# Kernel optimization log

Hardware: AMD Instinct MI355X
Metric: run time of the kernel (lower is better)

## Reference

```python
import math
import jax, jax.numpy as jnp
import numpy as np
from jax import lax

INPUT_SIZE = 736
PATCH_SIZE = 16
PATCH_LENGTH = 768
EMBED_DIM = 768
BATCH = 32
N_RINGS = INPUT_SIZE // 2  # 368 rings, equal_interval=1


def _precompute_gather(input_size=INPUT_SIZE, patch_length=PATCH_LENGTH):
    """Replicates the torch buffer construction: per-radius-ring pixel masks
    sorted by angle, fused with the per-ring linear (align_corners=True)
    resize to patch_length. Returns flat gather indices and lerp weights."""
    H = W = input_size
    yc = np.arange(H) - (H - 1) / 2.0
    xc = np.arange(W) - (W - 1) / 2.0
    yy, xx = np.meshgrid(yc, xc, indexing='ij')  # yy=row offset, xx=col offset
    radius = np.sqrt(xx ** 2 + yy ** 2)
    R = input_size // 2
    off = (W - 1) / 2.0
    j = np.arange(patch_length)
    idx0_all, idx1_all, w_all = [], [], []
    for low in range(R):
        high = low + 1
        m = (radius > low) & (radius <= high)
        ry, rx = np.nonzero(m)  # row-major order, same as torch .nonzero()
        # Faithful to torch quirk: unbind names (x, y) = (row-off, col-off)
        xv = ry - off
        yv = rx - off
        deg = np.arctan2(-yv, xv) * 180.0 / math.pi
        flat = ry * W + rx
        order = np.argsort(deg, kind='stable')
        flat = flat[order]
        L = len(flat)
        # F.interpolate(mode='linear', align_corners=True) to patch_length
        if L == 1:
            src = np.zeros(patch_length)
        else:
            src = j * (L - 1) / (patch_length - 1)
        i0 = np.clip(np.floor(src).astype(np.int64), 0, L - 1)
        i1 = np.minimum(i0 + 1, L - 1)
        wt = (src - i0).astype(np.float32)
        idx0_all.append(flat[i0])
        idx1_all.append(flat[i1])
        w_all.append(wt)
    idx0 = np.concatenate(idx0_all).astype(np.int32)
    idx1 = np.concatenate(idx1_all).astype(np.int32)
    w = np.concatenate(w_all).astype(np.float32)
    return idx0, idx1, w


def setup_inputs() -> dict:
    key = jax.random.key(0)
    k1, k2 = jax.random.split(key)
    x = jax.random.normal(k1, (BATCH, 3, INPUT_SIZE, INPUT_SIZE), dtype=jnp.float32)
    fan_in = 3 * PATCH_SIZE * PATCH_SIZE
    conv_w = jax.random.normal(k2, (EMBED_DIM, 3, PATCH_SIZE, PATCH_SIZE), dtype=jnp.float32) / np.sqrt(fan_in)
    conv_b = jnp.zeros((EMBED_DIM,), dtype=jnp.float32)
    idx0, idx1, w = _precompute_gather()
    return {
        'x': x,
        'conv_w': conv_w,
        'conv_b': conv_b,
        'idx0': jnp.asarray(idx0),
        'idx1': jnp.asarray(idx1),
        'w': jnp.asarray(w),
    }


def reference(x, conv_w, conv_b, idx0, idx1, w):
    N = x.shape[0]
    flat = x.reshape(N, 3, -1)  # [N, 3, H*W]
    # Fused irregular gather + per-ring linear resize (lerp between neighbors)
    g0 = flat[:, :, idx0]
    g1 = flat[:, :, idx1]
    patches = g0 * (1.0 - w) + g1 * w  # [N, 3, N_RINGS*PATCH_LENGTH]
    patches = patches.reshape(N, 3, N_RINGS, PATCH_LENGTH)  # [N,3,368,768]
    out = lax.conv_general_dilated(
        patches, conv_w,
        window_strides=(PATCH_SIZE, PATCH_SIZE),
        padding='VALID',
        dimension_numbers=('NCHW', 'OIHW', 'NCHW'),
    )
    return out + conv_b[None, :, None, None]  # [N, 768, 23, 48]
```

## Files before the change

### kernel.cpp

```cpp
#include <hip/hip_runtime.h>
#include <hip/hip_bf16.h>
#include <stdint.h>

#define INPUT_SIZE   736
#define PLANE_ELEMS  (736*736)
#define N_RINGS      368
#define PATCH_LEN    768
#define EMBED        768
#define BATCH        32
#define KDIM         768
#define M_TOTAL      (BATCH*23*48)
#define P_PER_BATCH  1104
#define OUT_BATCH_STRIDE 847872

typedef __bf16 bf16x8 __attribute__((ext_vector_type(8)));
typedef float  floatx4 __attribute__((ext_vector_type(4)));

__global__ void wcast_kernel(const float* __restrict__ wsrc,
                             __hip_bfloat16* __restrict__ Wb) {
    int i = blockIdx.x * 256 + threadIdx.x;
    Wb[i] = __float2bfloat16(wsrc[i]);
}

__global__ void gather_kernel(const float* __restrict__ x,
                              const int*   __restrict__ idx0,
                              const int*   __restrict__ idx1,
                              const float* __restrict__ w,
                              __hip_bfloat16* __restrict__ A) {
    int b    = blockIdx.x;
    int half = b & 1;
    int bb   = b >> 1;
    int band = bb % 23;
    int nc   = bb / 23;
    int c    = nc % 3;
    int n    = nc / 3;
    const float* plane = x + (size_t)nc * PLANE_ELEMS;

    int rr = threadIdx.x >> 4;
    int jj = threadIdx.x & 15;
    int r  = band * 16 + rr;
    int tbase = r * PATCH_LEN + jj + half * (24 * 16);
    size_t abase = ((size_t)(n * P_PER_BATCH + band * 48 + half * 24)) * KDIM
                 + c * 256 + threadIdx.x;

    #pragma unroll 8
    for (int jc = 0; jc < 24; jc++) {
        int t  = tbase + jc * 16;
        int i0 = idx0[t];
        int i1 = idx1[t];
        float wt = w[t];
        float v  = plane[i0] * (1.0f - wt) + plane[i1] * wt;
        A[abase + (size_t)jc * KDIM] = __float2bfloat16(v);
    }
}

__global__ __launch_bounds__(256) void gemm_kernel(
        const __hip_bfloat16* __restrict__ A,
        const __hip_bfloat16* __restrict__ Wb,
        const float* __restrict__ cb,
        float* __restrict__ out)
{
    __shared__ __hip_bfloat16 As[128 * 32];
    __shared__ __hip_bfloat16 Bs[128 * 32];

    const int tid  = threadIdx.x;
    const int lane = tid & 63;
    const int wv   = tid >> 6;
    const int wm   = wv & 1;
    const int wn   = wv >> 1;
    const int quad = lane >> 4;
    const int l16  = lane & 15;

    const int bn = blockIdx.x;
    const int bm = blockIdx.y;

    floatx4 acc[4][4];
    #pragma unroll
    for (int i = 0; i < 4; i++)
        #pragma unroll
        for (int j = 0; j < 4; j++)
            acc[i][j] = (floatx4){0.f, 0.f, 0.f, 0.f};

    const int srow = tid >> 2;
    const int kofs = (tid & 3) * 8;
    const __hip_bfloat16* aSrc = A  + (size_t)(bm * 128 + srow) * KDIM + kofs;
    const __hip_bfloat16* bSrc = Wb + (size_t)(bn * 128 + srow) * KDIM + kofs;
    __hip_bfloat16* aDst = As + tid * 8;
    __hip_bfloat16* bDst = Bs + tid * 8;

    for (int kt = 0; kt < 24; kt++) {
        const __hip_bfloat16* ap = aSrc + kt * 32;
        const __hip_bfloat16* bp = bSrc + kt * 32;
        __builtin_amdgcn_global_load_lds(
            (const __attribute__((address_space(1))) void*)(const void*)ap,
            (__attribute__((address_space(3))) void*)(void*)aDst, 16, 0, 0);
        __builtin_amdgcn_global_load_lds(
            (const __attribute__((address_space(1))) void*)(const void*)(ap + (size_t)64 * KDIM),
            (__attribute__((address_space(3))) void*)(void*)(aDst + 64 * 32), 16, 0, 0);
        __builtin_amdgcn_global_load_lds(
            (const __attribute__((address_space(1))) void*)(const void*)bp,
            (__attribute__((address_space(3))) void*)(void*)bDst, 16, 0, 0);
        __builtin_amdgcn_global_load_lds(
            (const __attribute__((address_space(1))) void*)(const void*)(bp + (size_t)64 * KDIM),
            (__attribute__((address_space(3))) void*)(void*)(bDst + 64 * 32), 16, 0, 0);
        __syncthreads();

        bf16x8 af[4], bfr[4];
        #pragma unroll
        for (int mi = 0; mi < 4; mi++) {
            int ml = wm * 64 + mi * 16 + l16;
            af[mi] = *(const bf16x8*)(As + ml * 32 + quad * 8);
        }
        #pragma unroll
        for (int ni = 0; ni < 4; ni++) {
            int el = wn * 64 + ni * 16 + l16;
            bfr[ni] = *(const bf16x8*)(Bs + el * 32 + quad * 8);
        }
        #pragma unroll
        for (int mi = 0; mi < 4; mi++)
            #pragma unroll
            for (int ni = 0; ni < 4; ni++)
                acc[mi][ni] = __builtin_amdgcn_mfma_f32_16x16x32_bf16(
                                  af[mi], bfr[ni], acc[mi][ni], 0, 0, 0);
        __syncthreads();
    }

    const int m0 = bm * 128 + wm * 64;
    const int e0 = bn * 128 + wn * 64;
    #pragma unroll
    for (int ni = 0; ni < 4; ni++) {
        int eg = e0 + ni * 16 + l16;
        float bias = cb[eg];
        #pragma unroll
        for (int mi = 0; mi < 4; mi++) {
            int mg = m0 + mi * 16 + quad * 4;
            int nb = mg / P_PER_BATCH;
            int p  = mg - nb * P_PER_BATCH;
            floatx4 v = acc[mi][ni];
            v[0] += bias; v[1] += bias; v[2] += bias; v[3] += bias;
            *(floatx4*)(out + (size_t)nb * OUT_BATCH_STRIDE
                            + (size_t)eg * P_PER_BATCH + p) = v;
        }
    }
}

extern "C" void kernel_launch(void* const* d_in, const int* in_sizes, int n_in,
                              void* d_out, int out_size, void* d_ws, size_t ws_size,
                              hipStream_t stream) {
    const float* x      = (const float*)d_in[0];
    const float* conv_w = (const float*)d_in[1];
    const float* conv_b = (const float*)d_in[2];
    const int*   idx0   = (const int*)  d_in[3];
    const int*   idx1   = (const int*)  d_in[4];
    const float* w      = (const float*)d_in[5];
    float* out = (float*)d_out;

    __hip_bfloat16* A  = (__hip_bfloat16*)d_ws;
    __hip_bfloat16* Wb = A + (size_t)M_TOTAL * KDIM;

    wcast_kernel<<<dim3(EMBED * KDIM / 256), dim3(256), 0, stream>>>(conv_w, Wb);

    gather_kernel<<<dim3(BATCH * 3 * (N_RINGS / 16) * 2), dim3(256), 0, stream>>>(
        x, idx0, idx1, w, A);

    gemm_kernel<<<dim3(EMBED / 128, M_TOTAL / 128), dim3(256), 0, stream>>>(
        A, Wb, conv_b, out);
}
```

Baseline: 444.4 us.

## Pack gather indices and weights into int2 and vectorize gather stores

Adds a pre-pass that packs idx0, the idx1-idx0 delta and a 16-bit quantized weight into one int2 per tap. The gather kernel then reads two taps per 16-byte load instead of three separate streams, and writes two bf16 values per store. This cuts index-metadata traffic, which repeats for every batch and channel. It adds an extra kernel launch and quantizes the lerp weight to 16 bits, a small accuracy change.

New measurement: 452.1 us. About the same (+1.7%).

```diff
diff --git a/kernel.cpp b/kernel.cpp
--- a/kernel.cpp
+++ b/kernel.cpp
@@ -12,9 +12,15 @@
 #define M_TOTAL      (BATCH*23*48)
 #define P_PER_BATCH  1104
 #define OUT_BATCH_STRIDE 847872
+#define GATHER_T     (N_RINGS*PATCH_LEN)
 
 typedef __bf16 bf16x8 __attribute__((ext_vector_type(8)));
 typedef float  floatx4 __attribute__((ext_vector_type(4)));
+
+static __device__ __forceinline__ unsigned short bf16bits(float f) {
+    __hip_bfloat16 h = __float2bfloat16(f);
+    return *reinterpret_cast<unsigned short*>(&h);
+}
 
 __global__ void wcast_kernel(const float* __restrict__ wsrc,
                              __hip_bfloat16* __restrict__ Wb) {
@@ -22,10 +28,20 @@
     Wb[i] = __float2bfloat16(wsrc[i]);
 }
 
+__global__ void pack_kernel(const int*   __restrict__ idx0,
+                            const int*   __restrict__ idx1,
+                            const float* __restrict__ w,
+                            int2* __restrict__ P) {
+    int t = blockIdx.x * 256 + threadIdx.x;
+    int i0 = idx0[t];
+    int d  = idx1[t] - i0;
+    unsigned w16 = (unsigned)(w[t] * 65536.0f);
+    if (w16 > 65535u) w16 = 65535u;
+    P[t] = make_int2(i0, (int)((w16 << 16) | ((unsigned)d & 0xFFFFu)));
+}
+
 __global__ void gather_kernel(const float* __restrict__ x,
-                              const int*   __restrict__ idx0,
-                              const int*   __restrict__ idx1,
-                              const float* __restrict__ w,
+                              const int2*  __restrict__ P,
                               __hip_bfloat16* __restrict__ A) {
     int b    = blockIdx.x;
     int half = b & 1;
@@ -39,18 +55,25 @@
     int rr = threadIdx.x >> 4;
     int jj = threadIdx.x & 15;
     int r  = band * 16 + rr;
-    int tbase = r * PATCH_LEN + jj + half * (24 * 16);
-    size_t abase = ((size_t)(n * P_PER_BATCH + band * 48 + half * 24)) * KDIM
-                 + c * 256 + threadIdx.x;
+    int tbase = r * PATCH_LEN + half * 384 + jj * 2;
 
-    #pragma unroll 8
-    for (int jc = 0; jc < 24; jc++) {
-        int t  = tbase + jc * 16;
-        int i0 = idx0[t];
-        int i1 = idx1[t];
-        float wt = w[t];
-        float v  = plane[i0] * (1.0f - wt) + plane[i1] * wt;
-        A[abase + (size_t)jc * KDIM] = __float2bfloat16(v);
+    int k = c * 256 + rr * 16 + (jj & 7) * 2;
+    size_t mbase = (size_t)(n * P_PER_BATCH + band * 48 + half * 24 + (jj >> 3));
+    __hip_bfloat16* aptr = A + mbase * KDIM + k;
+
+    #pragma unroll 4
+    for (int it = 0; it < 12; it++) {
+        int4 q = *reinterpret_cast<const int4*>(&P[tbase + it * 32]);
+        int   i0a = q.x;
+        int   i1a = i0a + (int)(short)((unsigned)q.y & 0xFFFFu);
+        float wa  = (float)((unsigned)q.y >> 16) * (1.0f / 65536.0f);
+        float va  = plane[i0a] * (1.0f - wa) + plane[i1a] * wa;
+        int   i0b = q.z;
+        int   i1b = i0b + (int)(short)((unsigned)q.w & 0xFFFFu);
+        float wb  = (float)((unsigned)q.w >> 16) * (1.0f / 65536.0f);
+        float vb  = plane[i0b] * (1.0f - wb) + plane[i1b] * wb;
+        *reinterpret_cast<ushort2*>(aptr + (size_t)(it * 2) * KDIM) =
+            make_ushort2(bf16bits(va), bf16bits(vb));
     }
 }
 
@@ -157,11 +180,14 @@
 
     __hip_bfloat16* A  = (__hip_bfloat16*)d_ws;
     __hip_bfloat16* Wb = A + (size_t)M_TOTAL * KDIM;
+    int2*           P  = (int2*)(Wb + (size_t)EMBED * KDIM);
 
     wcast_kernel<<<dim3(EMBED * KDIM / 256), dim3(256), 0, stream>>>(conv_w, Wb);
 
+    pack_kernel<<<dim3(GATHER_T / 256), dim3(256), 0, stream>>>(idx0, idx1, w, P);
+
     gather_kernel<<<dim3(BATCH * 3 * (N_RINGS / 16) * 2), dim3(256), 0, stream>>>(
-        x, idx0, idx1, w, A);
+        x, P, A);
 
     gemm_kernel<<<dim3(EMBED / 128, M_TOTAL / 128), dim3(256), 0, stream>>>(
         A, Wb, conv_b, out);
```

## Fuse ring gather and patch-embedding GEMM into one kernel via LDS

Applied to the files above, without the earlier changes.

Merges the gather/lerp kernel and the GEMM into one kernel. Each block owns one batch and one 16-row band, gathers its 48x768 A tile straight into swizzled LDS, then runs MFMA against bf16 weights read directly from global memory. This removes the write and re-read of the bf16 A matrix through HBM and one launch. The cost is only 736 blocks, 72 KB of LDS per block limiting occupancy, and B fragments loaded from global/L2 without LDS staging.

After: 477.2 us. 1.07x slower.

```diff
diff --git a/kernel.cpp b/kernel.cpp
--- a/kernel.cpp
+++ b/kernel.cpp
@@ -9,12 +9,16 @@
 #define EMBED        768
 #define BATCH        32
 #define KDIM         768
-#define M_TOTAL      (BATCH*23*48)
 #define P_PER_BATCH  1104
 #define OUT_BATCH_STRIDE 847872
 
 typedef __bf16 bf16x8 __attribute__((ext_vector_type(8)));
 typedef float  floatx4 __attribute__((ext_vector_type(4)));
+
+static __device__ __forceinline__ unsigned short bf16bits(float f) {
+    __hip_bfloat16 h = __float2bfloat16(f);
+    return *reinterpret_cast<unsigned short*>(&h);
+}
 
 __global__ void wcast_kernel(const float* __restrict__ wsrc,
                              __hip_bfloat16* __restrict__ Wb) {
@@ -22,124 +26,106 @@
     Wb[i] = __float2bfloat16(wsrc[i]);
 }
 
-__global__ void gather_kernel(const float* __restrict__ x,
-                              const int*   __restrict__ idx0,
-                              const int*   __restrict__ idx1,
-                              const float* __restrict__ w,
-                              __hip_bfloat16* __restrict__ A) {
-    int b    = blockIdx.x;
-    int half = b & 1;
-    int bb   = b >> 1;
-    int band = bb % 23;
-    int nc   = bb / 23;
-    int c    = nc % 3;
-    int n    = nc / 3;
-    const float* plane = x + (size_t)nc * PLANE_ELEMS;
-
-    int rr = threadIdx.x >> 4;
-    int jj = threadIdx.x & 15;
-    int r  = band * 16 + rr;
-    int tbase = r * PATCH_LEN + jj + half * (24 * 16);
-    size_t abase = ((size_t)(n * P_PER_BATCH + band * 48 + half * 24)) * KDIM
-                 + c * 256 + threadIdx.x;
-
-    #pragma unroll 8
-    for (int jc = 0; jc < 24; jc++) {
-        int t  = tbase + jc * 16;
-        int i0 = idx0[t];
-        int i1 = idx1[t];
-        float wt = w[t];
-        float v  = plane[i0] * (1.0f - wt) + plane[i1] * wt;
-        A[abase + (size_t)jc * KDIM] = __float2bfloat16(v);
-    }
-}
-
-__global__ __launch_bounds__(256) void gemm_kernel(
-        const __hip_bfloat16* __restrict__ A,
+__global__ __launch_bounds__(512, 4) void fused_kernel(
+        const float* __restrict__ x,
+        const int*   __restrict__ idx0,
+        const int*   __restrict__ idx1,
+        const float* __restrict__ w,
         const __hip_bfloat16* __restrict__ Wb,
         const float* __restrict__ cb,
         float* __restrict__ out)
 {
-    __shared__ __hip_bfloat16 As[128 * 32];
-    __shared__ __hip_bfloat16 Bs[128 * 32];
+    __shared__ __hip_bfloat16 Alds[48 * 768];
 
+    const int n    = blockIdx.x;
+    const int band = blockIdx.y;
     const int tid  = threadIdx.x;
+
+    {
+        const int rr    = tid & 15;
+        const int jslot = tid >> 4;
+        const int r     = band * 16 + rr;
+        const float* pl0 = x + (size_t)(n * 3 + 0) * PLANE_ELEMS;
+        const float* pl1 = x + (size_t)(n * 3 + 1) * PLANE_ELEMS;
+        const float* pl2 = x + (size_t)(n * 3 + 2) * PLANE_ELEMS;
+
+        #pragma unroll 2
+        for (int it = 0; it < 12; it++) {
+            const int j0 = jslot * 2 + it * 64;
+            const int t  = r * PATCH_LEN + j0;
+            int2   i0p = *(const int2*)(idx0 + t);
+            int2   i1p = *(const int2*)(idx1 + t);
+            float2 wp  = *(const float2*)(w + t);
+            const int pl  = j0 >> 4;
+            const int klo = j0 & 15;
+
+            #pragma unroll
+            for (int c = 0; c < 3; c++) {
+                const float* pp = (c == 0) ? pl0 : (c == 1) ? pl1 : pl2;
+                float va = pp[i0p.x] * (1.0f - wp.x) + pp[i1p.x] * wp.x;
+                float vb = pp[i0p.y] * (1.0f - wp.y) + pp[i1p.y] * wp.y;
+                const int k  = c * 256 + rr * 16 + klo;
+                const int s8 = k >> 3;
+                const int sw = (s8 & ~7) | ((s8 ^ pl) & 7);
+                *(ushort2*)((unsigned short*)Alds + pl * 768 + sw * 8 + (k & 7))
+                    = make_ushort2(bf16bits(va), bf16bits(vb));
+            }
+        }
+    }
+    __syncthreads();
+
     const int lane = tid & 63;
     const int wv   = tid >> 6;
-    const int wm   = wv & 1;
-    const int wn   = wv >> 1;
     const int quad = lane >> 4;
     const int l16  = lane & 15;
 
-    const int bn = blockIdx.x;
-    const int bm = blockIdx.y;
+    float* outBase = out + (size_t)n * OUT_BATCH_STRIDE + band * 48;
 
-    floatx4 acc[4][4];
     #pragma unroll
-    for (int i = 0; i < 4; i++)
+    for (int pass = 0; pass < 2; pass++) {
+        const int e0w = pass * 384 + wv * 48;
+
+        floatx4 acc[3][3];
         #pragma unroll
-        for (int j = 0; j < 4; j++)
-            acc[i][j] = (floatx4){0.f, 0.f, 0.f, 0.f};
+        for (int i = 0; i < 3; i++)
+            #pragma unroll
+            for (int j = 0; j < 3; j++)
+                acc[i][j] = (floatx4){0.f, 0.f, 0.f, 0.f};
 
-    const int srow = tid >> 2;
-    const int kofs = (tid & 3) * 8;
-    const __hip_bfloat16* aSrc = A  + (size_t)(bm * 128 + srow) * KDIM + kofs;
-    const __hip_bfloat16* bSrc = Wb + (size_t)(bn * 128 + srow) * KDIM + kofs;
-    __hip_bfloat16* aDst = As + tid * 8;
-    __hip_bfloat16* bDst = Bs + tid * 8;
+        #pragma unroll 2
+        for (int kt = 0; kt < 24; kt++) {
+            bf16x8 af[3], bfr[3];
+            const int s8 = kt * 4 + quad;
+            #pragma unroll
+            for (int mt = 0; mt < 3; mt++) {
+                const int row = mt * 16 + l16;
+                const int sw  = (s8 & ~7) | ((s8 ^ row) & 7);
+                af[mt] = *(const bf16x8*)(Alds + row * 768 + sw * 8);
+            }
+            #pragma unroll
+            for (int ni = 0; ni < 3; ni++) {
+                const int e = e0w + ni * 16 + l16;
+                bfr[ni] = *(const bf16x8*)(Wb + (size_t)e * KDIM + kt * 32 + quad * 8);
+            }
+            #pragma unroll
+            for (int mt = 0; mt < 3; mt++)
+                #pragma unroll
+                for (int ni = 0; ni < 3; ni++)
+                    acc[mt][ni] = __builtin_amdgcn_mfma_f32_16x16x32_bf16(
+                                      af[mt], bfr[ni], acc[mt][ni], 0, 0, 0);
+        }
 
-    for (int kt = 0; kt < 24; kt++) {
-        const __hip_bfloat16* ap = aSrc + kt * 32;
-        const __hip_bfloat16* bp = bSrc + kt * 32;
-        __builtin_amdgcn_global_load_lds(
-            (const __attribute__((address_space(1))) void*)(const void*)ap,
-            (__attribute__((address_space(3))) void*)(void*)aDst, 16, 0, 0);
-        __builtin_amdgcn_global_load_lds(
-            (const __attribute__((address_space(1))) void*)(const void*)(ap + (size_t)64 * KDIM),
-            (__attribute__((address_space(3))) void*)(void*)(aDst + 64 * 32), 16, 0, 0);
-        __builtin_amdgcn_global_load_lds(
-            (const __attribute__((address_space(1))) void*)(const void*)bp,
-            (__attribute__((address_space(3))) void*)(void*)bDst, 16, 0, 0);
-        __builtin_amdgcn_global_load_lds(
-            (const __attribute__((address_space(1))) void*)(const void*)(bp + (size_t)64 * KDIM),
-            (__attribute__((address_space(3))) void*)(void*)(bDst + 64 * 32), 16, 0, 0);
-        __syncthreads();
-
-        bf16x8 af[4], bfr[4];
         #pragma unroll
-        for (int mi = 0; mi < 4; mi++) {
-            int ml = wm * 64 + mi * 16 + l16;
-            af[mi] = *(const bf16x8*)(As + ml * 32 + quad * 8);
-        }
-        #pragma unroll
-        for (int ni = 0; ni < 4; ni++) {
-            int el = wn * 64 + ni * 16 + l16;
-            bfr[ni] = *(const bf16x8*)(Bs + el * 32 + quad * 8);
-        }
-        #pragma unroll
-        for (int mi = 0; mi < 4; mi++)
+        for (int ni = 0; ni < 3; ni++) {
+            const int eg = e0w + ni * 16 + l16;
+            const float bias = cb[eg];
             #pragma unroll
-            for (int ni = 0; ni < 4; ni++)
-                acc[mi][ni] = __builtin_amdgcn_mfma_f32_16x16x32_bf16(
-                                  af[mi], bfr[ni], acc[mi][ni], 0, 0, 0);
-        __syncthreads();
-    }
-
-    const int m0 = bm * 128 + wm * 64;
-    const int e0 = bn * 128 + wn * 64;
-    #pragma unroll
-    for (int ni = 0; ni < 4; ni++) {
-        int eg = e0 + ni * 16 + l16;
-        float bias = cb[eg];
-        #pragma unroll
-        for (int mi = 0; mi < 4; mi++) {
-            int mg = m0 + mi * 16 + quad * 4;
-            int nb = mg / P_PER_BATCH;
-            int p  = mg - nb * P_PER_BATCH;
-            floatx4 v = acc[mi][ni];
-            v[0] += bias; v[1] += bias; v[2] += bias; v[3] += bias;
-            *(floatx4*)(out + (size_t)nb * OUT_BATCH_STRIDE
-                            + (size_t)eg * P_PER_BATCH + p) = v;
+            for (int mt = 0; mt < 3; mt++) {
+                const int pl = mt * 16 + quad * 4;
+                floatx4 v = acc[mt][ni];
+                v[0] += bias; v[1] += bias; v[2] += bias; v[3] += bias;
+                *(floatx4*)(outBase + (size_t)eg * P_PER_BATCH + pl) = v;
+            }
         }
     }
 }
@@ -155,14 +141,10 @@
     const float* w      = (const float*)d_in[5];
     float* out = (float*)d_out;
 
-    __hip_bfloat16* A  = (__hip_bfloat16*)d_ws;
-    __hip_bfloat16* Wb = A + (size_t)M_TOTAL * KDIM;
+    __hip_bfloat16* Wb = (__hip_bfloat16*)d_ws;
 
     wcast_kernel<<<dim3(EMBED * KDIM / 256), dim3(256), 0, stream>>>(conv_w, Wb);
 
-    gather_kernel<<<dim3(BATCH * 3 * (N_RINGS / 16) * 2), dim3(256), 0, stream>>>(
-        x, idx0, idx1, w, A);
-
-    gemm_kernel<<<dim3(EMBED / 128, M_TOTAL / 128), dim3(256), 0, stream>>>(
-        A, Wb, conv_b, out);
+    fused_kernel<<<dim3(BATCH, 23), dim3(512), 0, stream>>>(
+        x, idx0, idx1, w, Wb, conv_b, out);
 }
```
